# Performance work log

Hardware: AMD Instinct MI355X
Metric: run time of the kernel (lower is better)

Reference implementation:

```python
import jax, jax.numpy as jnp
import numpy as np

B, S, E, H = 8, 1024, 1024, 16
D = E // H  # head_dim = 64


def setup_inputs() -> dict:
    key = jax.random.key(0)
    ks = jax.random.split(key, 10)
    def lin(k):
        kw, kb = jax.random.split(k)
        lim = 1.0 / np.sqrt(E)
        W = jax.random.uniform(kw, (E, E), jnp.float32, -lim, lim)
        b = jax.random.uniform(kb, (E,), jnp.float32, -lim, lim)
        return W, b
    Wq, bq = lin(ks[0]); Wk, bk = lin(ks[1]); Wv, bv = lin(ks[2]); Wo, bo = lin(ks[3])
    ent = jax.random.normal(ks[4], (H, H), jnp.float32)
    x = jax.random.normal(ks[5], (B, S, E), jnp.float32)
    mask = jnp.ones((B, 1, S, S), jnp.int32)
    return {"x": x, "mask": mask, "Wq": Wq, "bq": bq, "Wk": Wk, "bk": bk,
            "Wv": Wv, "bv": bv, "Wo": Wo, "bo": bo, "ent": ent}


def reference(x, mask, Wq, bq, Wk, bk, Wv, bv, Wo, bo, ent):
    Bs, Sl, Ed = x.shape
    def heads(W, b):
        return (x @ W.T + b).reshape(Bs, Sl, H, D).transpose(0, 2, 1, 3)  # [B,H,S,D]
    q, k, v = heads(Wq, bq), heads(Wk, bk), heads(Wv, bv)
    scores = jnp.einsum('bhqd,bhkd->bhqk', q, k) / np.sqrt(D)  # [B,H,S,S]
    Em = jax.nn.softmax(ent, axis=-1)  # [H,H]
    scores = jnp.einsum('bhqk,hg->bgqk', scores, Em)  # cross-head entanglement mix
    scores = jnp.where(mask == 0, jnp.float32(-1e9), scores)
    attn = jax.nn.softmax(scores, axis=-1)
    out = jnp.einsum('bhqk,bhkd->bhqd', attn, v)
    out = out.transpose(0, 2, 1, 3).reshape(Bs, Sl, Ed)
    return out @ Wo.T + bo
```

## Files before the change

kernel.cpp:

```cpp
#include <hip/hip_runtime.h>

#define DEVINL static __device__ __forceinline__

typedef __attribute__((ext_vector_type(4)))  float f32x4;
typedef __attribute__((ext_vector_type(16))) float f32x16;
typedef __attribute__((ext_vector_type(4)))  float float4_t;
typedef __attribute__((ext_vector_type(8)))  short short8;
typedef __attribute__((ext_vector_type(4)))  short short4v;
typedef __attribute__((ext_vector_type(4)))  int   int4v;

DEVINL unsigned short f2bf(float f){
  union { float f; unsigned int u; } x; x.f = f;
  return (unsigned short)((x.u + 0x7fffu + ((x.u >> 16) & 1u)) >> 16);
}
DEVINL float bf2f(unsigned short h){
  union { unsigned int u; float f; } x; x.u = ((unsigned int)h) << 16;
  return x.f;
}
DEVINL f32x4 zero4(){ f32x4 z; z[0]=0.f; z[1]=0.f; z[2]=0.f; z[3]=0.f; return z; }
DEVINL f32x16 zero16(){ f32x16 z;
#pragma unroll
  for (int e=0;e<16;++e) z[e]=0.f;
  return z; }

#define GLL16(gp, lp) __builtin_amdgcn_global_load_lds( \
    (const __attribute__((address_space(1))) void*)(gp), \
    (__attribute__((address_space(3))) void*)(lp), 16, 0, 0)

__global__ __launch_bounds__(256) void cast_f32_bf16(const float* __restrict__ src,
                                                     unsigned short* __restrict__ dst, int n8){
  int i = blockIdx.x * 256 + threadIdx.x;
  if (i >= n8) return;
  const float4_t* s = (const float4_t*)src;
  float4_t a = s[2*i], b = s[2*i+1];
  short8 o;
  o[0]=(short)f2bf(a[0]); o[1]=(short)f2bf(a[1]); o[2]=(short)f2bf(a[2]); o[3]=(short)f2bf(a[3]);
  o[4]=(short)f2bf(b[0]); o[5]=(short)f2bf(b[1]); o[6]=(short)f2bf(b[2]); o[7]=(short)f2bf(b[3]);
  *(short8*)(dst + (size_t)i*8) = o;
}

__global__ __launch_bounds__(256) void prep_em(const float* __restrict__ ent,
                                               unsigned short* __restrict__ EmT){
  int t = threadIdx.x;
  if (t < 16){
    float v[16]; float mx = -3.0e38f;
#pragma unroll
    for (int j=0;j<16;++j){ v[j] = ent[t*16 + j]; mx = fmaxf(mx, v[j]); }
    float s = 0.f;
#pragma unroll
    for (int j=0;j<16;++j){ v[j] = __expf(v[j]-mx); s += v[j]; }
    float inv = (1.f/s) * 0.125f * 1.4426950408889634f;
#pragma unroll
    for (int j=0;j<16;++j) EmT[j*16 + t] = f2bf(v[j]*inv);
  }
  EmT[256 + t] = 0;
}

template<int MODE>
__global__ __launch_bounds__(256) void gemm_bt(const unsigned short* __restrict__ A,
                                               const unsigned short* __restrict__ W4,
                                               const float* __restrict__ bias0,
                                               const float* __restrict__ bias1,
                                               const float* __restrict__ bias2,
                                               void* __restrict__ outp){
  __shared__ __align__(16) unsigned short As[4096];
  __shared__ __align__(16) unsigned short Bs[4096];
  const int tid = threadIdx.x;
  const int w = tid >> 6, ln = tid & 63;
  const int wm = w >> 1, wn = w & 1;
  const int lq = ln & 15, lg = ln >> 4;
  const int m0 = blockIdx.y * 128, n0 = blockIdx.x * 128;
  const int z = blockIdx.z;
  const unsigned short* Bt = W4 + (size_t)z * 1048576;
  const float* bias = (z == 0) ? bias0 : ((z == 1) ? bias1 : bias2);

  const unsigned short* Ag = A  + (size_t)(m0 + (tid >> 2)) * 1024 + (tid & 3) * 8;
  const unsigned short* Bg = Bt + (size_t)(n0 + (tid >> 2)) * 1024 + (tid & 3) * 8;
  unsigned short* lA0 = As + w * 512;
  unsigned short* lA1 = As + 2048 + w * 512;
  unsigned short* lB0 = Bs + w * 512;
  unsigned short* lB1 = Bs + 2048 + w * 512;

  f32x4 acc[4][4];
#pragma unroll
  for (int i=0;i<4;++i)
#pragma unroll
    for (int j=0;j<4;++j) acc[i][j] = zero4();

  for (int kb = 0; kb < 32; ++kb){
    const int k0 = kb * 32;
    GLL16(Ag + k0,         lA0);
    GLL16(Ag + k0 + 65536, lA1);
    GLL16(Bg + k0,         lB0);
    GLL16(Bg + k0 + 65536, lB1);
    __syncthreads();
    short8 af[4], bf_[4];
#pragma unroll
    for (int i=0;i<4;++i) af[i]  = *(const short8*)(As + (wm*64 + i*16 + lq)*32 + lg*8);
#pragma unroll
    for (int j=0;j<4;++j) bf_[j] = *(const short8*)(Bs + (wn*64 + j*16 + lq)*32 + lg*8);
#pragma unroll
    for (int i=0;i<4;++i)
#pragma unroll
      for (int j=0;j<4;++j)
        acc[i][j] = __builtin_amdgcn_mfma_f32_16x16x32_bf16(af[i], bf_[j], acc[i][j], 0, 0, 0);
    __syncthreads();
  }

  const int mrow = m0 + wm*64, ncol = n0 + wn*64;
  float bj[4];
#pragma unroll
  for (int j=0;j<4;++j) bj[j] = bias[ncol + j*16 + lq];
#pragma unroll
  for (int i=0;i<4;++i)
#pragma unroll
    for (int j=0;j<4;++j)
#pragma unroll
      for (int r=0;r<4;++r){
        float v = acc[i][j][r] + bj[j];
        int m = mrow + i*16 + lg*4 + r;
        int n = ncol + j*16 + lq;
        if (MODE == 0){
          int bb = m >> 10, sI = m & 1023, h = n >> 6, d = n & 63;
          ((unsigned short*)outp)[(size_t)z*8388608 + (((size_t)bb*16 + h)*1024 + sI)*64 + d] = f2bf(v);
        } else {
          ((float*)outp)[(size_t)m*1024 + n] = v;
        }
      }
}

__global__ __launch_bounds__(256) void transpose_v(const unsigned short* __restrict__ V,
                                                   unsigned short* __restrict__ Vt){
  int idx = blockIdx.x * 256 + threadIdx.x;
  int s8 = idx & 127, d = (idx >> 7) & 63, bh = idx >> 13;
  const unsigned short* src = V + (size_t)bh*65536 + (size_t)s8*8*64 + d;
  short8 o;
#pragma unroll
  for (int j=0;j<8;++j) o[j] = (short)src[(size_t)j*64];
  *(short8*)(Vt + (size_t)bh*65536 + (size_t)d*1024 + (size_t)s8*8) = o;
}

__global__ __launch_bounds__(512) void attn_fused(const unsigned short* __restrict__ Q,
    const unsigned short* __restrict__ K, const unsigned short* __restrict__ Vt,
    const int* __restrict__ mask, const unsigned short* __restrict__ EmT,
    unsigned short* __restrict__ AO){
  __shared__ __align__(16) unsigned short sraw[16384];
  __shared__ __align__(16) unsigned short smix[16384];
  const int tid = threadIdx.x;
  const int w = tid >> 6, ln = tid & 63;
  const int lq = ln & 15, lg = ln >> 4;
  const int l5 = ln & 31, h5 = ln >> 5;
  const int bb = blockIdx.y, q0 = blockIdx.x * 32;
  const int aQ = w & 3, iw = w >> 2, g0 = w * 2;

  const unsigned short* Qb = Q  + ((size_t)bb*16 + 4*aQ) * 65536;
  const unsigned short* Kb = K  + ((size_t)bb*16 + 4*aQ) * 65536;
  const unsigned short* Vb = Vt + ((size_t)bb*16 + g0) * 65536;
  const int* Mb = mask + (size_t)bb*1048576 + (size_t)q0*1024;

  short8 emA = *(const short8*)(EmT + l5*16 + h5*8);

  short8 qf[4][2];
#pragma unroll
  for (int hh=0; hh<4; ++hh)
#pragma unroll
    for (int ks=0; ks<2; ++ks)
      qf[hh][ks] = *(const short8*)(Qb + (size_t)hh*65536 + (size_t)(q0 + iw*16 + lq)*64 + ks*32 + lg*8);

  f32x4 acco[2][2][4];
#pragma unroll
  for (int a=0;a<2;++a)
#pragma unroll
    for (int i=0;i<2;++i)
#pragma unroll
      for (int n=0;n<4;++n) acco[a][i][n] = zero4();
  float mst[2][2] = {{-3.0e38f,-3.0e38f},{-3.0e38f,-3.0e38f}};
  float lst[2][2] = {{0.f,0.f},{0.f,0.f}};

  for (int kt = 0; kt < 32; ++kt){
    const int kb = kt*32;
    f32x4 accs[4][2];
#pragma unroll
    for (int hh=0;hh<4;++hh){ accs[hh][0] = zero4(); accs[hh][1] = zero4(); }
    short8 kf[2][2][2];
#pragma unroll
    for (int n=0;n<2;++n)
#pragma unroll
      for (int ks=0;ks<2;++ks)
        kf[0][n][ks] = *(const short8*)(Kb + (size_t)(kb + n*16 + lq)*64 + ks*32 + lg*8);
#pragma unroll
    for (int hh=0; hh<4; ++hh){
      if (hh < 3){
#pragma unroll
        for (int n=0;n<2;++n)
#pragma unroll
          for (int ks=0;ks<2;++ks)
            kf[(hh+1)&1][n][ks] = *(const short8*)(Kb + (size_t)(hh+1)*65536 + (size_t)(kb + n*16 + lq)*64 + ks*32 + lg*8);
      }
#pragma unroll
      for (int n=0;n<2;++n)
#pragma unroll
        for (int ks=0;ks<2;++ks)
          accs[hh][n] = __builtin_amdgcn_mfma_f32_16x16x32_bf16(qf[hh][ks], kf[hh&1][n][ks], accs[hh][n], 0,0,0);
    }
#pragma unroll
    for (int n=0;n<2;++n)
#pragma unroll
      for (int r=0;r<4;++r){
        const int qq = iw*16 + lg*4 + r;
        const int kk = n*16 + lq;
        short4v pk;
        pk[0]=(short)f2bf(accs[0][n][r]); pk[1]=(short)f2bf(accs[1][n][r]);
        pk[2]=(short)f2bf(accs[2][n][r]); pk[3]=(short)f2bf(accs[3][n][r]);
        const int lin = (qq*32 + kk)*32 + aQ*8;
        const int sw  = (((kk>>2)&1)<<4) | (((qq>>2)&3)<<5);
        *(short4v*)((char*)sraw + (lin ^ sw)) = pk;
      }
    __syncthreads();
    short8 sfr[4];
#pragma unroll
    for (int t=0;t<4;++t){
      const int qq = w*4 + t;
      const int lin = (qq*32 + l5)*32 + h5*16;
      const int sw  = (((l5>>2)&1)<<4) | (((qq>>2)&3)<<5);
      sfr[t] = *(const short8*)((const char*)sraw + (lin ^ sw));
    }
#pragma unroll
    for (int t=0;t<4;++t){
      const int qq = w*4 + t;
      f32x16 md = __builtin_amdgcn_mfma_f32_32x32x16_bf16(emA, sfr[t], zero16(), 0,0,0);
#pragma unroll
      for (int reg=0;reg<8;++reg){
        const int gg = (reg&3) + 8*(reg>>2) + 4*h5;
        const int lin = (gg*32 + qq)*64 + l5*2;
        const int sw  = ((gg>>2)&1)<<6;
        *(short*)((char*)smix + (lin ^ sw)) = (short)f2bf(md[reg]);
      }
    }
    __syncthreads();
#pragma unroll
    for (int hh=0; hh<2; ++hh){
      const int gg = g0 + hh;
      const int sw6 = ((gg>>2)&1)<<6;
#pragma unroll
      for (int i=0;i<2;++i){
        const int qq = i*16 + lq;
        short8 sm8 = *(const short8*)((const char*)smix + ((((gg*32 + qq)*64) + lg*16) ^ sw6));
        short8 vfr[4];
#pragma unroll
        for (int n=0;n<4;++n)
          vfr[n] = *(const short8*)(Vb + (size_t)hh*65536 + (size_t)(n*16 + lq)*1024 + kb + lg*8);
        const int4v mv0 = *(const int4v*)(Mb + (size_t)qq*1024 + kb + lg*8);
        const int4v mv1 = *(const int4v*)(Mb + (size_t)qq*1024 + kb + lg*8 + 4);
        float s[8];
#pragma unroll
        for (int j=0;j<8;++j) s[j] = bf2f((unsigned short)sm8[j]);
#pragma unroll
        for (int j=0;j<4;++j){
          if (mv0[j]==0) s[j]   = -1.44269504e9f;
          if (mv1[j]==0) s[4+j] = -1.44269504e9f;
        }
        float pm = s[0];
#pragma unroll
        for (int j=1;j<8;++j) pm = fmaxf(pm, s[j]);
        pm = fmaxf(pm, __shfl_xor(pm, 16, 64));
        pm = fmaxf(pm, __shfl_xor(pm, 32, 64));
        const float mo = mst[hh][i];
        const float mn = fmaxf(mo, pm);
        const float sc = exp2f(mo - mn);
        float p[8]; float ps = 0.f;
#pragma unroll
        for (int j=0;j<8;++j){ p[j] = exp2f(s[j] - mn); ps += p[j]; }
        ps += __shfl_xor(ps, 16, 64);
        ps += __shfl_xor(ps, 32, 64);
        lst[hh][i] = lst[hh][i]*sc + ps;
        mst[hh][i] = mn;
        short8 pa;
#pragma unroll
        for (int j=0;j<8;++j) pa[j] = (short)f2bf(p[j]);
        const float scr0 = __shfl(sc, lg*4 + 0, 64);
        const float scr1 = __shfl(sc, lg*4 + 1, 64);
        const float scr2 = __shfl(sc, lg*4 + 2, 64);
        const float scr3 = __shfl(sc, lg*4 + 3, 64);
#pragma unroll
        for (int n=0;n<4;++n){
          acco[hh][i][n][0] *= scr0; acco[hh][i][n][1] *= scr1;
          acco[hh][i][n][2] *= scr2; acco[hh][i][n][3] *= scr3;
        }
#pragma unroll
        for (int n=0;n<4;++n)
          acco[hh][i][n] = __builtin_amdgcn_mfma_f32_16x16x32_bf16(pa, vfr[n], acco[hh][i][n], 0,0,0);
      }
    }
  }
#pragma unroll
  for (int hh=0; hh<2; ++hh){
    const int gg = g0 + hh;
#pragma unroll
    for (int i=0;i<2;++i){
      const float linv = 1.0f / lst[hh][i];
      const float l0 = __shfl(linv, lg*4+0, 64), l1 = __shfl(linv, lg*4+1, 64);
      const float l2 = __shfl(linv, lg*4+2, 64), l3 = __shfl(linv, lg*4+3, 64);
#pragma unroll
      for (int n=0;n<4;++n){
        const int e = gg*64 + n*16 + lq;
        const size_t base = ((size_t)bb*1024 + (size_t)(q0 + i*16 + lg*4))*1024 + e;
        AO[base         ] = f2bf(acco[hh][i][n][0]*l0);
        AO[base + 1024  ] = f2bf(acco[hh][i][n][1]*l1);
        AO[base + 2048  ] = f2bf(acco[hh][i][n][2]*l2);
        AO[base + 3072  ] = f2bf(acco[hh][i][n][3]*l3);
      }
    }
  }
}

extern "C" void kernel_launch(void* const* d_in, const int* in_sizes, int n_in,
                              void* d_out, int out_size, void* d_ws, size_t ws_size,
                              hipStream_t stream){
  const float* x   = (const float*)d_in[0];
  const int*   msk = (const int*)  d_in[1];
  const float* Wq  = (const float*)d_in[2];
  const float* bq  = (const float*)d_in[3];
  const float* Wk  = (const float*)d_in[4];
  const float* bk  = (const float*)d_in[5];
  const float* Wv  = (const float*)d_in[6];
  const float* bv  = (const float*)d_in[7];
  const float* Wo  = (const float*)d_in[8];
  const float* bo  = (const float*)d_in[9];
  const float* ent = (const float*)d_in[10];

  char* ws = (char*)d_ws;
  unsigned short* xb  = (unsigned short*)(ws);
  unsigned short* Wb  = (unsigned short*)(ws + 16777216);
  unsigned short* qkv = (unsigned short*)(ws + 25165824);
  unsigned short* EmT = (unsigned short*)(ws + 75497472);
  unsigned short* Vt  = xb;
  unsigned short* AO  = qkv + (size_t)2*8388608;

  cast_f32_bf16<<<4096, 256, 0, stream>>>(x,  xb,            1048576);
  cast_f32_bf16<<<512,  256, 0, stream>>>(Wq, Wb,            131072);
  cast_f32_bf16<<<512,  256, 0, stream>>>(Wk, Wb + 1048576,  131072);
  cast_f32_bf16<<<512,  256, 0, stream>>>(Wv, Wb + 2097152,  131072);
  cast_f32_bf16<<<512,  256, 0, stream>>>(Wo, Wb + 3145728,  131072);
  prep_em<<<1, 256, 0, stream>>>(ent, EmT);

  gemm_bt<0><<<dim3(8,64,3), 256, 0, stream>>>(xb, Wb, bq, bk, bv, (void*)qkv);
  transpose_v<<<4096, 256, 0, stream>>>(qkv + (size_t)2*8388608, Vt);
  attn_fused<<<dim3(32,8,1), 512, 0, stream>>>(qkv, qkv + 8388608, Vt, msk, EmT, AO);
  gemm_bt<1><<<dim3(8,64,1), 256, 0, stream>>>(AO, Wb + 3145728, bo, bo, bo, d_out);

  (void)in_sizes; (void)n_in; (void)out_size; (void)ws_size;
}
```

Measured before the change: 430.2 us.

## Halve attention query tile, pack mask to bits, skip masking when all-ones

The attention kernel now processes 16 queries per block instead of 32, launching 512 blocks rather than 256. This halves shared memory and registers per block and sets launch bounds to allow more resident blocks, aimed at better occupancy and CU fill. A new pre-pass packs the int32 mask into a bitmask, cutting mask traffic by 32x. Each wave also skips the per-element masking when all of its mask bits are set. The cost is an extra kernel launch, and K/Q fragments are reloaded by twice as many blocks.

```diff
diff --git a/kernel.cpp b/kernel.cpp
--- a/kernel.cpp
+++ b/kernel.cpp
@@ -54,6 +54,22 @@
     for (int j=0;j<16;++j) EmT[j*16 + t] = f2bf(v[j]*inv);
   }
   EmT[256 + t] = 0;
+}
+
+__global__ __launch_bounds__(256) void prep_maskbits(const int* __restrict__ mask,
+                                                     unsigned* __restrict__ mb){
+  int id = blockIdx.x * 256 + threadIdx.x;
+  const int* src = mask + (size_t)id * 32;
+  unsigned word = 0u;
+#pragma unroll
+  for (int c=0;c<8;++c){
+    int4v v = *(const int4v*)(src + c*4);
+    word |= (unsigned)(v[0]!=0) << (c*4)
+          | (unsigned)(v[1]!=0) << (c*4+1)
+          | (unsigned)(v[2]!=0) << (c*4+2)
+          | (unsigned)(v[3]!=0) << (c*4+3);
+  }
+  mb[id] = word;
 }
 
 template<int MODE>
@@ -140,23 +156,24 @@
   *(short8*)(Vt + (size_t)bh*65536 + (size_t)d*1024 + (size_t)s8*8) = o;
 }
 
-__global__ __launch_bounds__(512) void attn_fused(const unsigned short* __restrict__ Q,
+__global__ __launch_bounds__(512,4) void attn_fused(const unsigned short* __restrict__ Q,
     const unsigned short* __restrict__ K, const unsigned short* __restrict__ Vt,
-    const int* __restrict__ mask, const unsigned short* __restrict__ EmT,
+    const unsigned* __restrict__ MB, const unsigned short* __restrict__ EmT,
     unsigned short* __restrict__ AO){
-  __shared__ __align__(16) unsigned short sraw[16384];
-  __shared__ __align__(16) unsigned short smix[16384];
+  __shared__ __align__(16) unsigned short sraw[8192];
+  __shared__ __align__(16) unsigned short smix[8192];
   const int tid = threadIdx.x;
   const int w = tid >> 6, ln = tid & 63;
   const int lq = ln & 15, lg = ln >> 4;
   const int l5 = ln & 31, h5 = ln >> 5;
-  const int bb = blockIdx.y, q0 = blockIdx.x * 32;
-  const int aQ = w & 3, iw = w >> 2, g0 = w * 2;
+  const int bid = blockIdx.x;
+  const int bb = bid & 7, q0 = (bid >> 3) * 16;
+  const int aQ = w & 3, n0 = w >> 2, g0 = w * 2;
 
   const unsigned short* Qb = Q  + ((size_t)bb*16 + 4*aQ) * 65536;
-  const unsigned short* Kb = K  + ((size_t)bb*16 + 4*aQ) * 65536;
+  const unsigned short* Kb = K  + ((size_t)bb*16 + 4*aQ) * 65536 + (size_t)(n0*16 + lq)*64 + lg*8;
   const unsigned short* Vb = Vt + ((size_t)bb*16 + g0) * 65536;
-  const int* Mb = mask + (size_t)bb*1048576 + (size_t)q0*1024;
+  const unsigned* Mw = MB + (size_t)bb*32768 + (size_t)(q0 + lq)*32;
 
   short8 emA = *(const short8*)(EmT + l5*16 + h5*8);
 
@@ -165,151 +182,120 @@
   for (int hh=0; hh<4; ++hh)
 #pragma unroll
     for (int ks=0; ks<2; ++ks)
-      qf[hh][ks] = *(const short8*)(Qb + (size_t)hh*65536 + (size_t)(q0 + iw*16 + lq)*64 + ks*32 + lg*8);
-
-  f32x4 acco[2][2][4];
+      qf[hh][ks] = *(const short8*)(Qb + (size_t)hh*65536 + (size_t)(q0 + lq)*64 + ks*32 + lg*8);
+
+  f32x4 acco[2][4];
 #pragma unroll
   for (int a=0;a<2;++a)
 #pragma unroll
-    for (int i=0;i<2;++i)
-#pragma unroll
-      for (int n=0;n<4;++n) acco[a][i][n] = zero4();
-  float mst[2][2] = {{-3.0e38f,-3.0e38f},{-3.0e38f,-3.0e38f}};
-  float lst[2][2] = {{0.f,0.f},{0.f,0.f}};
+    for (int n=0;n<4;++n) acco[a][n] = zero4();
+  float mst[2] = {-3.0e38f,-3.0e38f};
+  float lst[2] = {0.f,0.f};
+
+  const int kk = n0*16 + lq;
 
   for (int kt = 0; kt < 32; ++kt){
     const int kb = kt*32;
-    f32x4 accs[4][2];
-#pragma unroll
-    for (int hh=0;hh<4;++hh){ accs[hh][0] = zero4(); accs[hh][1] = zero4(); }
-    short8 kf[2][2][2];
-#pragma unroll
-    for (int n=0;n<2;++n)
-#pragma unroll
-      for (int ks=0;ks<2;++ks)
-        kf[0][n][ks] = *(const short8*)(Kb + (size_t)(kb + n*16 + lq)*64 + ks*32 + lg*8);
+    f32x4 accs[4];
 #pragma unroll
     for (int hh=0; hh<4; ++hh){
-      if (hh < 3){
-#pragma unroll
-        for (int n=0;n<2;++n)
-#pragma unroll
-          for (int ks=0;ks<2;++ks)
-            kf[(hh+1)&1][n][ks] = *(const short8*)(Kb + (size_t)(hh+1)*65536 + (size_t)(kb + n*16 + lq)*64 + ks*32 + lg*8);
-      }
-#pragma unroll
-      for (int n=0;n<2;++n)
-#pragma unroll
-        for (int ks=0;ks<2;++ks)
-          accs[hh][n] = __builtin_amdgcn_mfma_f32_16x16x32_bf16(qf[hh][ks], kf[hh&1][n][ks], accs[hh][n], 0,0,0);
-    }
-#pragma unroll
-    for (int n=0;n<2;++n)
-#pragma unroll
-      for (int r=0;r<4;++r){
-        const int qq = iw*16 + lg*4 + r;
-        const int kk = n*16 + lq;
-        short4v pk;
-        pk[0]=(short)f2bf(accs[0][n][r]); pk[1]=(short)f2bf(accs[1][n][r]);
-        pk[2]=(short)f2bf(accs[2][n][r]); pk[3]=(short)f2bf(accs[3][n][r]);
-        const int lin = (qq*32 + kk)*32 + aQ*8;
-        const int sw  = (((kk>>2)&1)<<4) | (((qq>>2)&3)<<5);
-        *(short4v*)((char*)sraw + (lin ^ sw)) = pk;
-      }
+      short8 k0 = *(const short8*)(Kb + (size_t)hh*65536 + (size_t)kb*64);
+      short8 k1 = *(const short8*)(Kb + (size_t)hh*65536 + (size_t)kb*64 + 32);
+      accs[hh] = __builtin_amdgcn_mfma_f32_16x16x32_bf16(qf[hh][0], k0, zero4(), 0,0,0);
+      accs[hh] = __builtin_amdgcn_mfma_f32_16x16x32_bf16(qf[hh][1], k1, accs[hh], 0,0,0);
+    }
+#pragma unroll
+    for (int r=0;r<4;++r){
+      const int qq = lg*4 + r;
+      short4v pk;
+      pk[0]=(short)f2bf(accs[0][r]); pk[1]=(short)f2bf(accs[1][r]);
+      pk[2]=(short)f2bf(accs[2][r]); pk[3]=(short)f2bf(accs[3][r]);
+      const int lin = (qq*32 + kk)*32 + aQ*8;
+      const int sw  = (((kk>>2)&1)<<4) | (((qq>>2)&3)<<5);
+      *(short4v*)((char*)sraw + (lin ^ sw)) = pk;
+    }
     __syncthreads();
-    short8 sfr[4];
-#pragma unroll
-    for (int t=0;t<4;++t){
-      const int qq = w*4 + t;
+#pragma unroll
+    for (int t=0;t<2;++t){
+      const int qq = w*2 + t;
       const int lin = (qq*32 + l5)*32 + h5*16;
       const int sw  = (((l5>>2)&1)<<4) | (((qq>>2)&3)<<5);
-      sfr[t] = *(const short8*)((const char*)sraw + (lin ^ sw));
-    }
-#pragma unroll
-    for (int t=0;t<4;++t){
-      const int qq = w*4 + t;
-      f32x16 md = __builtin_amdgcn_mfma_f32_32x32x16_bf16(emA, sfr[t], zero16(), 0,0,0);
+      short8 sfr = *(const short8*)((const char*)sraw + (lin ^ sw));
+      f32x16 md = __builtin_amdgcn_mfma_f32_32x32x16_bf16(emA, sfr, zero16(), 0,0,0);
 #pragma unroll
       for (int reg=0;reg<8;++reg){
         const int gg = (reg&3) + 8*(reg>>2) + 4*h5;
-        const int lin = (gg*32 + qq)*64 + l5*2;
-        const int sw  = ((gg>>2)&1)<<6;
-        *(short*)((char*)smix + (lin ^ sw)) = (short)f2bf(md[reg]);
+        int ob = gg*1024 + qq*64 + l5*2;
+        ob ^= ((gg>>2)&1)<<6;
+        *(short*)((char*)smix + ob) = (short)f2bf(md[reg]);
       }
     }
     __syncthreads();
+    const unsigned mw = Mw[kt];
+    const unsigned mshift = mw >> (lg*8);
+    const int allon = __all((int)((mshift & 0xffu) == 0xffu));
 #pragma unroll
     for (int hh=0; hh<2; ++hh){
       const int gg = g0 + hh;
-      const int sw6 = ((gg>>2)&1)<<6;
-#pragma unroll
-      for (int i=0;i<2;++i){
-        const int qq = i*16 + lq;
-        short8 sm8 = *(const short8*)((const char*)smix + ((((gg*32 + qq)*64) + lg*16) ^ sw6));
-        short8 vfr[4];
-#pragma unroll
-        for (int n=0;n<4;++n)
-          vfr[n] = *(const short8*)(Vb + (size_t)hh*65536 + (size_t)(n*16 + lq)*1024 + kb + lg*8);
-        const int4v mv0 = *(const int4v*)(Mb + (size_t)qq*1024 + kb + lg*8);
-        const int4v mv1 = *(const int4v*)(Mb + (size_t)qq*1024 + kb + lg*8 + 4);
-        float s[8];
-#pragma unroll
-        for (int j=0;j<8;++j) s[j] = bf2f((unsigned short)sm8[j]);
-#pragma unroll
-        for (int j=0;j<4;++j){
-          if (mv0[j]==0) s[j]   = -1.44269504e9f;
-          if (mv1[j]==0) s[4+j] = -1.44269504e9f;
-        }
-        float pm = s[0];
-#pragma unroll
-        for (int j=1;j<8;++j) pm = fmaxf(pm, s[j]);
-        pm = fmaxf(pm, __shfl_xor(pm, 16, 64));
-        pm = fmaxf(pm, __shfl_xor(pm, 32, 64));
-        const float mo = mst[hh][i];
-        const float mn = fmaxf(mo, pm);
-        const float sc = exp2f(mo - mn);
-        float p[8]; float ps = 0.f;
-#pragma unroll
-        for (int j=0;j<8;++j){ p[j] = exp2f(s[j] - mn); ps += p[j]; }
-        ps += __shfl_xor(ps, 16, 64);
-        ps += __shfl_xor(ps, 32, 64);
-        lst[hh][i] = lst[hh][i]*sc + ps;
-        mst[hh][i] = mn;
-        short8 pa;
-#pragma unroll
-        for (int j=0;j<8;++j) pa[j] = (short)f2bf(p[j]);
-        const float scr0 = __shfl(sc, lg*4 + 0, 64);
-        const float scr1 = __shfl(sc, lg*4 + 1, 64);
-        const float scr2 = __shfl(sc, lg*4 + 2, 64);
-        const float scr3 = __shfl(sc, lg*4 + 3, 64);
-#pragma unroll
-        for (int n=0;n<4;++n){
-          acco[hh][i][n][0] *= scr0; acco[hh][i][n][1] *= scr1;
-          acco[hh][i][n][2] *= scr2; acco[hh][i][n][3] *= scr3;
-        }
-#pragma unroll
-        for (int n=0;n<4;++n)
-          acco[hh][i][n] = __builtin_amdgcn_mfma_f32_16x16x32_bf16(pa, vfr[n], acco[hh][i][n], 0,0,0);
+      const int rb = (gg*1024 + lq*64 + lg*16) ^ (((gg>>2)&1)<<6);
+      short8 sm8 = *(const short8*)((const char*)smix + rb);
+      short8 vfr[4];
+#pragma unroll
+      for (int n=0;n<4;++n)
+        vfr[n] = *(const short8*)(Vb + (size_t)hh*65536 + (size_t)(n*16 + lq)*1024 + kb + lg*8);
+      float s[8];
+#pragma unroll
+      for (int j=0;j<8;++j) s[j] = bf2f((unsigned short)sm8[j]);
+      if (!allon){
+#pragma unroll
+        for (int j=0;j<8;++j) if (!((mshift>>j)&1u)) s[j] = -1.44269504e9f;
       }
+      float pm = s[0];
+#pragma unroll
+      for (int j=1;j<8;++j) pm = fmaxf(pm, s[j]);
+      pm = fmaxf(pm, __shfl_xor(pm, 16, 64));
+      pm = fmaxf(pm, __shfl_xor(pm, 32, 64));
+      const float mo = mst[hh];
+      const float mn = fmaxf(mo, pm);
+      const float sc = exp2f(mo - mn);
+      float p[8]; float ps = 0.f;
+#pragma unroll
+      for (int j=0;j<8;++j){ p[j] = exp2f(s[j] - mn); ps += p[j]; }
+      ps += __shfl_xor(ps, 16, 64);
+      ps += __shfl_xor(ps, 32, 64);
+      lst[hh] = lst[hh]*sc + ps;
+      mst[hh] = mn;
+      short8 pa;
+#pragma unroll
+      for (int j=0;j<8;++j) pa[j] = (short)f2bf(p[j]);
+      const float scr0 = __shfl(sc, lg*4 + 0, 64);
+      const float scr1 = __shfl(sc, lg*4 + 1, 64);
+      const float scr2 = __shfl(sc, lg*4 + 2, 64);
+      const float scr3 = __shfl(sc, lg*4 + 3, 64);
+#pragma unroll
+      for (int n=0;n<4;++n){
+        acco[hh][n][0] *= scr0; acco[hh][n][1] *= scr1;
+        acco[hh][n][2] *= scr2; acco[hh][n][3] *= scr3;
+      }
+#pragma unroll
+      for (int n=0;n<4;++n)
+        acco[hh][n] = __builtin_amdgcn_mfma_f32_16x16x32_bf16(pa, vfr[n], acco[hh][n], 0,0,0);
     }
   }
 #pragma unroll
   for (int hh=0; hh<2; ++hh){
     const int gg = g0 + hh;
-#pragma unroll
-    for (int i=0;i<2;++i){
-      const float linv = 1.0f / lst[hh][i];
-      const float l0 = __shfl(linv, lg*4+0, 64), l1 = __shfl(linv, lg*4+1, 64);
-      const float l2 = __shfl(linv, lg*4+2, 64), l3 = __shfl(linv, lg*4+3, 64);
-#pragma unroll
-      for (int n=0;n<4;++n){
-        const int e = gg*64 + n*16 + lq;
-        const size_t base = ((size_t)bb*1024 + (size_t)(q0 + i*16 + lg*4))*1024 + e;
-        AO[base         ] = f2bf(acco[hh][i][n][0]*l0);
-        AO[base + 1024  ] = f2bf(acco[hh][i][n][1]*l1);
-        AO[base + 2048  ] = f2bf(acco[hh][i][n][2]*l2);
-        AO[base + 3072  ] = f2bf(acco[hh][i][n][3]*l3);
-      }
+    const float linv = 1.0f / lst[hh];
+    const float l0 = __shfl(linv, lg*4+0, 64), l1 = __shfl(linv, lg*4+1, 64);
+    const float l2 = __shfl(linv, lg*4+2, 64), l3 = __shfl(linv, lg*4+3, 64);
+#pragma unroll
+    for (int n=0;n<4;++n){
+      const int e = gg*64 + n*16 + lq;
+      const size_t base = ((size_t)bb*1024 + (size_t)(q0 + lg*4))*1024 + e;
+      AO[base         ] = f2bf(acco[hh][n][0]*l0);
+      AO[base + 1024  ] = f2bf(acco[hh][n][1]*l1);
+      AO[base + 2048  ] = f2bf(acco[hh][n][2]*l2);
+      AO[base + 3072  ] = f2bf(acco[hh][n][3]*l3);
     }
   }
 }
@@ -334,6 +320,7 @@
   unsigned short* Wb  = (unsigned short*)(ws + 16777216);
   unsigned short* qkv = (unsigned short*)(ws + 25165824);
   unsigned short* EmT = (unsigned short*)(ws + 75497472);
+  unsigned*       MB  = (unsigned*)     (ws + 75499520);
   unsigned short* Vt  = xb;
   unsigned short* AO  = qkv + (size_t)2*8388608;
 
@@ -343,10 +330,11 @@
   cast_f32_bf16<<<512,  256, 0, stream>>>(Wv, Wb + 2097152,  131072);
   cast_f32_bf16<<<512,  256, 0, stream>>>(Wo, Wb + 3145728,  131072);
   prep_em<<<1, 256, 0, stream>>>(ent, EmT);
+  prep_maskbits<<<1024, 256, 0, stream>>>(msk, MB);
 
   gemm_bt<0><<<dim3(8,64,3), 256, 0, stream>>>(xb, Wb, bq, bk, bv, (void*)qkv);
   transpose_v<<<4096, 256, 0, stream>>>(qkv + (size_t)2*8388608, Vt);
-  attn_fused<<<dim3(32,8,1), 512, 0, stream>>>(qkv, qkv + 8388608, Vt, msk, EmT, AO);
+  attn_fused<<<512, 512, 0, stream>>>(qkv, qkv + 8388608, Vt, MB, EmT, AO);
   gemm_bt<1><<<dim3(8,64,1), 256, 0, stream>>>(AO, Wb + 3145728, bo, bo, bo, d_out);
 
   (void)in_sizes; (void)n_in; (void)out_size; (void)ws_size;
```

Result: slower. 496.8 us (+15.5%).
